# Performance work log

Hardware: AMD Instinct MI355X
Metric: run time of the kernel (lower is better)

The kernel has to match this reference:

```python
import jax, jax.numpy as jnp
import numpy as np

N = 50000      # nodes
E = 800000     # edges (avg degree 16)
G = 500        # graphs in batch
D = 128        # emb_dim
ED = 7         # edge_dim
L = 5          # num_layers
C = 10         # num_class
BN_EPS = 1e-5


def _bn(x, g, b, m, v):
    # BatchNorm1d in eval mode: running stats
    return (x - m) * jax.lax.rsqrt(v + BN_EPS) * g + b


def setup_inputs() -> dict:
    key = jax.random.key(0)
    ks = jax.random.split(key, 32)
    f32 = jnp.float32
    edge_attr = jax.random.normal(ks[0], (E, ED), f32)
    edge_index = jax.random.randint(ks[1], (2, E), 0, N)
    batch = jnp.sort(jax.random.randint(ks[2], (N,), 0, G))

    w = lambda k, shp, s: jax.random.normal(k, shp, f32) * s
    s_in = 1.0 / np.sqrt(D)
    node_emb = w(ks[3], (1, D), 1.0)
    edge_W = w(ks[4], (L, ED, D), 1.0 / np.sqrt(ED))
    edge_b = w(ks[5], (L, D), 0.01)
    mlp_W1 = w(ks[6], (L, D, D), s_in)
    mlp_b1 = w(ks[7], (L, D), 0.01)
    mlp_W2 = w(ks[8], (L, D, D), s_in)
    mlp_b2 = w(ks[9], (L, D), 0.01)
    bn1_g = jax.random.uniform(ks[10], (L, D), f32, 0.5, 1.5)
    bn1_b = w(ks[11], (L, D), 0.1)
    bn1_m = w(ks[12], (L, D), 0.1)
    bn1_v = jax.random.uniform(ks[13], (L, D), f32, 0.5, 1.5)
    bn2_g = jax.random.uniform(ks[14], (L, D), f32, 0.5, 1.5)
    bn2_b = w(ks[15], (L, D), 0.1)
    bn2_m = w(ks[16], (L, D), 0.1)
    bn2_v = jax.random.uniform(ks[17], (L, D), f32, 0.5, 1.5)
    head_W1 = w(ks[18], (D, D), s_in)
    head_b1 = w(ks[19], (D,), 0.01)
    head_W2 = w(ks[20], (D, C), s_in)
    head_b2 = w(ks[21], (C,), 0.01)
    return dict(edge_attr=edge_attr, edge_index=edge_index, batch=batch,
                node_emb=node_emb, edge_W=edge_W, edge_b=edge_b,
                mlp_W1=mlp_W1, mlp_b1=mlp_b1, bn1_g=bn1_g, bn1_b=bn1_b,
                bn1_m=bn1_m, bn1_v=bn1_v, mlp_W2=mlp_W2, mlp_b2=mlp_b2,
                bn2_g=bn2_g, bn2_b=bn2_b, bn2_m=bn2_m, bn2_v=bn2_v,
                head_W1=head_W1, head_b1=head_b1, head_W2=head_W2, head_b2=head_b2)


def reference(edge_attr, edge_index, batch, node_emb, edge_W, edge_b,
              mlp_W1, mlp_b1, bn1_g, bn1_b, bn1_m, bn1_v,
              mlp_W2, mlp_b2, bn2_g, bn2_b, bn2_m, bn2_v,
              head_W1, head_b1, head_W2, head_b2):
    src, dst = edge_index[0], edge_index[1]
    # node_emb indexed by zeros -> every node starts with the same row
    x = jnp.broadcast_to(node_emb[0], (N, D))
    for l in range(L):
        # GINEConv: msg_ij = relu(x_j + Lin(edge_attr_ij)); aggr = sum over in-edges
        e = edge_attr @ edge_W[l] + edge_b[l]               # [E, D]
        msg = jax.nn.relu(x[src] + e)                       # gather + add + relu
        agg = jax.ops.segment_sum(msg, dst, num_segments=N) # scatter-add
        h = x + agg                                         # (1 + eps) * x, eps = 0
        # inner MLP: Linear -> BN -> ReLU -> Linear
        h = h @ mlp_W1[l] + mlp_b1[l]
        h = jax.nn.relu(_bn(h, bn1_g[l], bn1_b[l], bn1_m[l], bn1_v[l]))
        h = h @ mlp_W2[l] + mlp_b2[l]
        # outer BN + ReLU (dropout identity in eval)
        x = jax.nn.relu(_bn(h, bn2_g[l], bn2_b[l], bn2_m[l], bn2_v[l]))
    # global mean pool over graphs
    counts = jnp.maximum(jax.ops.segment_sum(jnp.ones((N,), x.dtype), batch, num_segments=G), 1.0)
    g = jax.ops.segment_sum(x, batch, num_segments=G) / counts[:, None]
    # head: Linear -> ReLU -> (Dropout) -> Linear
    h = jax.nn.relu(g @ head_W1 + head_b1)
    return h @ head_W2 + head_b2
```

## Files before the change

kernel.cpp:

```cpp
#include <hip/hip_runtime.h>

#define N_NODES 50000
#define N_PAD   50048
#define N_EDGES 800000
#define N_GRAPHS 500
#define DIM 128
#define EDIM 7
#define LAYERS 5
#define NCLASS 10
#define BN_EPS 1e-5f
#define TM 64
#define AST 264
#define NSB ((N_NODES + 256) / 256)

typedef __attribute__((ext_vector_type(8))) short bf16x8;
typedef __attribute__((ext_vector_type(4))) float f32x4;
typedef _Float16 h2 __attribute__((ext_vector_type(2)));

__device__ __forceinline__ unsigned short f2bf(float f) {
    unsigned u = __float_as_uint(f);
    u = u + 0x7fffu + ((u >> 16) & 1u);
    return (unsigned short)(u >> 16);
}
__device__ __forceinline__ float bf2f(unsigned short h) {
    return __uint_as_float(((unsigned)h) << 16);
}
__device__ __forceinline__ h2 u2h2(unsigned u) {
    union { unsigned u; h2 h; } c; c.u = u; return c.h;
}
__device__ __forceinline__ unsigned h22u(h2 h) {
    union { h2 h; unsigned u; } c; c.h = h; return c.u;
}
__device__ __forceinline__ unsigned packh2(float a, float b) {
    h2 h; h.x = (_Float16)a; h.y = (_Float16)b;
    return h22u(h);
}


__global__ void zero_ints(int* __restrict__ p, int n) {
    int i = blockIdx.x * 256 + threadIdx.x;
    if (i < n) p[i] = 0;
}

__global__ void hist_kernel(const int* __restrict__ dst, int* __restrict__ deg) {
    int e = blockIdx.x * 256 + threadIdx.x;
    if (e < N_EDGES) atomicAdd(&deg[dst[e]], 1);
}

__global__ __launch_bounds__(256)
void scan1(const int* __restrict__ deg, int* __restrict__ ro, int* __restrict__ bsums) {
    __shared__ int ws[4];
    int t = threadIdx.x;
    int i = blockIdx.x * 256 + t;
    int v = (i < N_NODES) ? deg[i] : 0;
    int lane = t & 63, wv = t >> 6;
    int s = v;
    #pragma unroll
    for (int off = 1; off < 64; off <<= 1) {
        int u = __shfl_up(s, off, 64);
        if (lane >= off) s += u;
    }
    if (lane == 63) ws[wv] = s;
    __syncthreads();
    if (t == 0) {
        int a = 0;
        #pragma unroll
        for (int k = 0; k < 4; ++k) { int x = ws[k]; ws[k] = a; a += x; }
        bsums[blockIdx.x] = a;
    }
    __syncthreads();
    int excl = s - v + ws[wv];
    if (i <= N_NODES) ro[i] = excl;
}

__global__ __launch_bounds__(256)
void scan2(int* __restrict__ bsums) {
    __shared__ int ws[4];
    int t = threadIdx.x;
    int v = (t < NSB) ? bsums[t] : 0;
    int lane = t & 63, wv = t >> 6;
    int s = v;
    #pragma unroll
    for (int off = 1; off < 64; off <<= 1) {
        int u = __shfl_up(s, off, 64);
        if (lane >= off) s += u;
    }
    if (lane == 63) ws[wv] = s;
    __syncthreads();
    if (t == 0) {
        int a = 0;
        #pragma unroll
        for (int k = 0; k < 4; ++k) { int x = ws[k]; ws[k] = a; a += x; }
    }
    __syncthreads();
    if (t < NSB) bsums[t] = s - v + ws[wv];
}

__global__ __launch_bounds__(256)
void scan3(int* __restrict__ ro, const int* __restrict__ bsums, int* __restrict__ cursor) {
    int i = blockIdx.x * 256 + threadIdx.x;
    if (i <= N_NODES) {
        int r = ro[i] + bsums[i >> 8];
        ro[i] = r;
        if (i < N_NODES) cursor[i] = r;
    }
}

__global__ void fill_csr(const int* __restrict__ dst, int* __restrict__ cursor,
                         int* __restrict__ csr_edges) {
    int e = blockIdx.x * 256 + threadIdx.x;
    if (e < N_EDGES) {
        int pos = atomicAdd(&cursor[dst[e]], 1);
        csr_edges[pos] = e;
    }
}


__global__ void init_x(float* __restrict__ x, unsigned short* __restrict__ xb,
                       const float* __restrict__ emb) {
    int i = blockIdx.x * 256 + threadIdx.x;
    if (i < N_NODES * DIM) {
        float v = emb[i & (DIM - 1)];
        x[i] = v;
        xb[i] = f2bf(v);
    }
}

__global__ void prep_ea(const float* __restrict__ ea, _Float16* __restrict__ eah) {
    int i = blockIdx.x * 256 + threadIdx.x;
    if (i < N_EDGES * 8) {
        int e = i >> 3, k = i & 7;
        float v = (k < EDIM) ? ea[e * EDIM + k] : 0.f;
        eah[i] = (_Float16)v;
    }
}

__global__ void prep_w(const float* __restrict__ W1, const float* __restrict__ W2,
                       unsigned short* __restrict__ Wthi, unsigned short* __restrict__ Wtlo) {
    int i = blockIdx.x * 256 + threadIdx.x;
    if (i >= 2 * LAYERS * DIM * DIM) return;
    int m = i >> 14;
    int n = i & 127;
    int k = (i >> 7) & 127;
    const float* W = (m < LAYERS) ? (W1 + (size_t)m * DIM * DIM)
                                  : (W2 + (size_t)(m - LAYERS) * DIM * DIM);
    float v = W[k * DIM + n];
    unsigned short hi = f2bf(v);
    float lo = v - bf2f(hi);
    size_t o = ((size_t)m << 14) + (size_t)n * DIM + k;
    Wthi[o] = hi;
    Wtlo[o] = f2bf(lo);
}


#if __has_builtin(__builtin_amdgcn_fdot2)
#define HAVE_FDOT2 1
#else
#define HAVE_FDOT2 0
#endif

__device__ __forceinline__ void edge_accum(float4& acc, uint4 eav, uint2 xv,
                                           const unsigned* Wp, const float4& bd) {
    float4 el = bd;
#if HAVE_FDOT2
    #pragma unroll
    for (int d = 0; d < 4; ++d) {
        float e = (d == 0) ? el.x : (d == 1) ? el.y : (d == 2) ? el.z : el.w;
        e = __builtin_amdgcn_fdot2(u2h2(eav.x), u2h2(Wp[d * 4 + 0]), e, false);
        e = __builtin_amdgcn_fdot2(u2h2(eav.y), u2h2(Wp[d * 4 + 1]), e, false);
        e = __builtin_amdgcn_fdot2(u2h2(eav.z), u2h2(Wp[d * 4 + 2]), e, false);
        e = __builtin_amdgcn_fdot2(u2h2(eav.w), u2h2(Wp[d * 4 + 3]), e, false);
        if (d == 0) el.x = e; else if (d == 1) el.y = e; else if (d == 2) el.z = e; else el.w = e;
    }
#else
    h2 ea01 = u2h2(eav.x), ea23 = u2h2(eav.y), ea45 = u2h2(eav.z), ea67 = u2h2(eav.w);
    float a[8] = {(float)ea01.x, (float)ea01.y, (float)ea23.x, (float)ea23.y,
                  (float)ea45.x, (float)ea45.y, (float)ea67.x, 0.f};
    #pragma unroll
    for (int d = 0; d < 4; ++d) {
        float e = (d == 0) ? el.x : (d == 1) ? el.y : (d == 2) ? el.z : el.w;
        #pragma unroll
        for (int kp = 0; kp < 4; ++kp) {
            h2 w = u2h2(Wp[d * 4 + kp]);
            e += a[kp * 2] * (float)w.x + a[kp * 2 + 1] * (float)w.y;
        }
        if (d == 0) el.x = e; else if (d == 1) el.y = e; else if (d == 2) el.z = e; else el.w = e;
    }
#endif
    acc.x += fmaxf(__uint_as_float(xv.x << 16)         + el.x, 0.f);
    acc.y += fmaxf(__uint_as_float(xv.x & 0xffff0000u) + el.y, 0.f);
    acc.z += fmaxf(__uint_as_float(xv.y << 16)         + el.z, 0.f);
    acc.w += fmaxf(__uint_as_float(xv.y & 0xffff0000u) + el.w, 0.f);
}

__global__ __launch_bounds__(256, 4)
void aggregate(const float* __restrict__ x, const unsigned short* __restrict__ xb,
               float* __restrict__ h,
               const _Float16* __restrict__ eah,
               const int* __restrict__ srcA,
               const int* __restrict__ csr,
               const int* __restrict__ row_off,
               const float* __restrict__ eW, const float* __restrict__ eb) {
    int t = threadIdx.x;
    int nl = t >> 5, lane = t & 31, c0 = lane * 4;
    int n = blockIdx.x * 8 + nl;

    unsigned Wp[16];
    #pragma unroll
    for (int d = 0; d < 4; ++d) {
        #pragma unroll
        for (int kp = 0; kp < 4; ++kp) {
            float w0 = eW[(kp * 2) * DIM + c0 + d];
            float w1 = (kp * 2 + 1 < EDIM) ? eW[(kp * 2 + 1) * DIM + c0 + d] : 0.f;
            Wp[d * 4 + kp] = packh2(w0, w1);
        }
    }
    float4 bd = *reinterpret_cast<const float4*>(eb + c0);
    #pragma unroll
    for (int k = 0; k < 16; ++k) asm volatile("" : "+v"(Wp[k]));
    asm volatile("" : "+v"(bd.x), "+v"(bd.y), "+v"(bd.z), "+v"(bd.w));

    float4 acc = *reinterpret_cast<const float4*>(x + (size_t)n * DIM + c0);
    int idx = row_off[n], end = row_off[n + 1];

    int e_c[4], s_c[4];
    bool have = (idx + 4 <= end);
    if (have) {
        #pragma unroll
        for (int j = 0; j < 4; ++j) e_c[j] = csr[idx + j];
        #pragma unroll
        for (int j = 0; j < 4; ++j) s_c[j] = srcA[e_c[j]];
    }
    while (have) {
        uint4 ea[4]; uint2 xv[4];
        #pragma unroll
        for (int j = 0; j < 4; ++j) ea[j] = *reinterpret_cast<const uint4*>(eah + (size_t)e_c[j] * 8);
        #pragma unroll
        for (int j = 0; j < 4; ++j) xv[j] = *reinterpret_cast<const uint2*>(xb + (size_t)s_c[j] * DIM + c0);
        idx += 4;
        bool nxt = (idx + 4 <= end);
        int e_n[4], s_n[4];
        if (nxt) {
            #pragma unroll
            for (int j = 0; j < 4; ++j) e_n[j] = csr[idx + j];
            #pragma unroll
            for (int j = 0; j < 4; ++j) s_n[j] = srcA[e_n[j]];
        }
        #pragma unroll
        for (int j = 0; j < 4; ++j) edge_accum(acc, ea[j], xv[j], Wp, bd);
        if (nxt) {
            #pragma unroll
            for (int j = 0; j < 4; ++j) { e_c[j] = e_n[j]; s_c[j] = s_n[j]; }
        }
        have = nxt;
    }
    for (; idx < end; ++idx) {
        int e = csr[idx];
        int s = srcA[e];
        uint4 ea = *reinterpret_cast<const uint4*>(eah + (size_t)e * 8);
        uint2 xv = *reinterpret_cast<const uint2*>(xb + (size_t)s * DIM + c0);
        edge_accum(acc, ea, xv, Wp, bd);
    }
    *reinterpret_cast<float4*>(h + (size_t)n * DIM + c0) = acc;
}


__global__ __launch_bounds__(256)
void gemm2x(const float* __restrict__ in, float* __restrict__ outx,
            unsigned short* __restrict__ xb_out,
            const unsigned short* __restrict__ W1hi, const unsigned short* __restrict__ W1lo,
            const unsigned short* __restrict__ W2hi, const unsigned short* __restrict__ W2lo,
            const float* __restrict__ b1,
            const float* __restrict__ bn1g, const float* __restrict__ bn1b,
            const float* __restrict__ bn1m, const float* __restrict__ bn1v,
            const float* __restrict__ b2,
            const float* __restrict__ bn2g, const float* __restrict__ bn2b,
            const float* __restrict__ bn2m, const float* __restrict__ bn2v) {
    __shared__ __align__(16) unsigned short A2[TM * AST];
    int t = threadIdx.x;
    int r0 = blockIdx.x * TM;
    int w = t >> 6;
    int lane = t & 63;
    int q = lane >> 4;
    int l16 = lane & 15;

    bf16x8 bh[2][4], bl[2][4];
    #pragma unroll
    for (int nt = 0; nt < 2; ++nt) {
        int n = w * 32 + nt * 16 + l16;
        const bf16x8* gh = reinterpret_cast<const bf16x8*>(W1hi + (size_t)n * DIM);
        const bf16x8* gl = reinterpret_cast<const bf16x8*>(W1lo + (size_t)n * DIM);
        #pragma unroll
        for (int kc = 0; kc < 4; ++kc) {
            bh[nt][kc] = gh[kc * 4 + q];
            bl[nt][kc] = gl[kc * 4 + q];
        }
    }

    #pragma unroll
    for (int i = 0; i < 8; ++i) {
        int idx = t + i * 256;
        int row = idx >> 5;
        int kp = (idx & 31) * 4;
        float4 v = reinterpret_cast<const float4*>(in + (size_t)r0 * DIM)[idx];
        unsigned short h0 = f2bf(v.x), h1 = f2bf(v.y), h2_ = f2bf(v.z), h3 = f2bf(v.w);
        ushort4 hv; hv.x = h0; hv.y = h1; hv.z = h2_; hv.w = h3;
        ushort4 lv;
        lv.x = f2bf(v.x - bf2f(h0)); lv.y = f2bf(v.y - bf2f(h1));
        lv.z = f2bf(v.z - bf2f(h2_)); lv.w = f2bf(v.w - bf2f(h3));
        *reinterpret_cast<ushort4*>(&A2[row * AST + kp]) = hv;
        *reinterpret_cast<ushort4*>(&A2[row * AST + 128 + kp]) = lv;
    }
    __syncthreads();

    f32x4 acc[4][2];
    #pragma unroll
    for (int mt = 0; mt < 4; ++mt)
        #pragma unroll
        for (int nt = 0; nt < 2; ++nt)
            acc[mt][nt] = (f32x4){0.f, 0.f, 0.f, 0.f};

    #pragma unroll
    for (int kc = 0; kc < 4; ++kc) {
        bf16x8 ahi[4], alo[4];
        #pragma unroll
        for (int mt = 0; mt < 4; ++mt) {
            ahi[mt] = *reinterpret_cast<const bf16x8*>(&A2[(mt * 16 + l16) * AST + kc * 32 + q * 8]);
            alo[mt] = *reinterpret_cast<const bf16x8*>(&A2[(mt * 16 + l16) * AST + 128 + kc * 32 + q * 8]);
        }
        #pragma unroll
        for (int mt = 0; mt < 4; ++mt)
            #pragma unroll
            for (int nt = 0; nt < 2; ++nt) {
                acc[mt][nt] = __builtin_amdgcn_mfma_f32_16x16x32_bf16(ahi[mt], bh[nt][kc], acc[mt][nt], 0, 0, 0);
                acc[mt][nt] = __builtin_amdgcn_mfma_f32_16x16x32_bf16(ahi[mt], bl[nt][kc], acc[mt][nt], 0, 0, 0);
                acc[mt][nt] = __builtin_amdgcn_mfma_f32_16x16x32_bf16(alo[mt], bh[nt][kc], acc[mt][nt], 0, 0, 0);
            }
    }
    __syncthreads();

    #pragma unroll
    for (int nt = 0; nt < 2; ++nt) {
        int col = w * 32 + nt * 16 + l16;
        float bias = b1[col];
        float sc = bn1g[col] * rsqrtf(bn1v[col] + BN_EPS);
        float sh = bn1b[col] - bn1m[col] * sc;
        #pragma unroll
        for (int mt = 0; mt < 4; ++mt) {
            #pragma unroll
            for (int r = 0; r < 4; ++r) {
                int rowl = mt * 16 + q * 4 + r;
                float o = fmaxf((acc[mt][nt][r] + bias) * sc + sh, 0.f);
                unsigned short hi = f2bf(o);
                A2[rowl * AST + col] = hi;
                A2[rowl * AST + 128 + col] = f2bf(o - bf2f(hi));
            }
        }
    }

    #pragma unroll
    for (int nt = 0; nt < 2; ++nt) {
        int n = w * 32 + nt * 16 + l16;
        const bf16x8* gh = reinterpret_cast<const bf16x8*>(W2hi + (size_t)n * DIM);
        const bf16x8* gl = reinterpret_cast<const bf16x8*>(W2lo + (size_t)n * DIM);
        #pragma unroll
        for (int kc = 0; kc < 4; ++kc) {
            bh[nt][kc] = gh[kc * 4 + q];
            bl[nt][kc] = gl[kc * 4 + q];
        }
    }
    __syncthreads();

    #pragma unroll
    for (int mt = 0; mt < 4; ++mt)
        #pragma unroll
        for (int nt = 0; nt < 2; ++nt)
            acc[mt][nt] = (f32x4){0.f, 0.f, 0.f, 0.f};

    #pragma unroll
    for (int kc = 0; kc < 4; ++kc) {
        bf16x8 ahi[4], alo[4];
        #pragma unroll
        for (int mt = 0; mt < 4; ++mt) {
            ahi[mt] = *reinterpret_cast<const bf16x8*>(&A2[(mt * 16 + l16) * AST + kc * 32 + q * 8]);
            alo[mt] = *reinterpret_cast<const bf16x8*>(&A2[(mt * 16 + l16) * AST + 128 + kc * 32 + q * 8]);
        }
        #pragma unroll
        for (int mt = 0; mt < 4; ++mt)
            #pragma unroll
            for (int nt = 0; nt < 2; ++nt) {
                acc[mt][nt] = __builtin_amdgcn_mfma_f32_16x16x32_bf16(ahi[mt], bh[nt][kc], acc[mt][nt], 0, 0, 0);
                acc[mt][nt] = __builtin_amdgcn_mfma_f32_16x16x32_bf16(ahi[mt], bl[nt][kc], acc[mt][nt], 0, 0, 0);
                acc[mt][nt] = __builtin_amdgcn_mfma_f32_16x16x32_bf16(alo[mt], bh[nt][kc], acc[mt][nt], 0, 0, 0);
            }
    }

    #pragma unroll
    for (int nt = 0; nt < 2; ++nt) {
        int col = w * 32 + nt * 16 + l16;
        float bias = b2[col];
        float sc = bn2g[col] * rsqrtf(bn2v[col] + BN_EPS);
        float sh = bn2b[col] - bn2m[col] * sc;
        #pragma unroll
        for (int mt = 0; mt < 4; ++mt) {
            #pragma unroll
            for (int r = 0; r < 4; ++r) {
                int row = r0 + mt * 16 + q * 4 + r;
                float o = fmaxf((acc[mt][nt][r] + bias) * sc + sh, 0.f);
                outx[(size_t)row * DIM + col] = o;
                xb_out[(size_t)row * DIM + col] = f2bf(o);
            }
        }
    }
}


__global__ __launch_bounds__(256)
void pool_kernel(const float* __restrict__ x, const int* __restrict__ batch,
                 float* __restrict__ g) {
    __shared__ float sh[256];
    __shared__ int sb[2];
    int gid = blockIdx.x;
    int t = threadIdx.x;
    if (t < 2) {
        int tgt = gid + t;
        int lo = 0, hi = N_NODES;
        while (lo < hi) { int mid = (lo + hi) >> 1; if (batch[mid] < tgt) lo = mid + 1; else hi = mid; }
        sb[t] = lo;
    }
    __syncthreads();
    int lo = sb[0], hi = sb[1];
    int d = t & 127, half = t >> 7;
    float a = 0.f;
    for (int n = lo + half; n < hi; n += 2) a += x[(size_t)n * DIM + d];
    sh[t] = a;
    __syncthreads();
    if (t < DIM) {
        float cnt = fmaxf((float)(hi - lo), 1.f);
        g[gid * DIM + t] = (sh[t] + sh[t + 128]) / cnt;
    }
}


__global__ __launch_bounds__(128)
void head1_kernel(const float* __restrict__ g, const float* __restrict__ W1,
                  const float* __restrict__ b1, float* __restrict__ h1) {
    __shared__ float gs[DIM];
    int gid = blockIdx.x, c = threadIdx.x;
    gs[c] = g[gid * DIM + c];
    __syncthreads();
    float acc = b1[c];
    for (int k = 0; k < DIM; ++k) acc += gs[k] * W1[k * DIM + c];
    h1[gid * DIM + c] = fmaxf(acc, 0.f);
}

__global__ __launch_bounds__(64)
void head2_kernel(const float* __restrict__ h1, const float* __restrict__ W2,
                  const float* __restrict__ b2, float* __restrict__ out) {
    __shared__ float hs[DIM];
    int gid = blockIdx.x;
    int t = threadIdx.x;
    hs[t] = h1[gid * DIM + t];
    hs[t + 64] = h1[gid * DIM + t + 64];
    __syncthreads();
    if (t < NCLASS) {
        float acc = b2[t];
        for (int k = 0; k < DIM; ++k) acc += hs[k] * W2[k * NCLASS + t];
        out[gid * NCLASS + t] = acc;
    }
}


extern "C" void kernel_launch(void* const* d_in, const int* in_sizes, int n_in,
                              void* d_out, int out_size, void* d_ws, size_t ws_size,
                              hipStream_t stream) {
    const float* edge_attr = (const float*)d_in[0];
    const int*   edge_index = (const int*)d_in[1];
    const int*   batch = (const int*)d_in[2];
    const float* node_emb = (const float*)d_in[3];
    const float* edge_W = (const float*)d_in[4];
    const float* edge_b = (const float*)d_in[5];
    const float* mlp_W1 = (const float*)d_in[6];
    const float* mlp_b1 = (const float*)d_in[7];
    const float* bn1_g = (const float*)d_in[8];
    const float* bn1_b = (const float*)d_in[9];
    const float* bn1_m = (const float*)d_in[10];
    const float* bn1_v = (const float*)d_in[11];
    const float* mlp_W2 = (const float*)d_in[12];
    const float* mlp_b2 = (const float*)d_in[13];
    const float* bn2_g = (const float*)d_in[14];
    const float* bn2_b = (const float*)d_in[15];
    const float* bn2_m = (const float*)d_in[16];
    const float* bn2_v = (const float*)d_in[17];
    const float* head_W1 = (const float*)d_in[18];
    const float* head_b1 = (const float*)d_in[19];
    const float* head_W2 = (const float*)d_in[20];
    const float* head_b2 = (const float*)d_in[21];
    float* out = (float*)d_out;

    const int* src = edge_index;
    const int* dst = edge_index + N_EDGES;

    size_t off = 0;
    auto carve = [&](size_t bytes) {
        void* p = (char*)d_ws + off;
        off += (bytes + 255) & ~(size_t)255;
        return p;
    };
    float* x            = (float*)carve((size_t)N_PAD * DIM * 4);
    unsigned short* xb  = (unsigned short*)carve((size_t)N_PAD * DIM * 2);
    float* h            = (float*)carve((size_t)N_PAD * DIM * 4);
    _Float16* eah       = (_Float16*)carve((size_t)N_EDGES * 8 * 2);
    unsigned short* Wthi = (unsigned short*)carve((size_t)2 * LAYERS * DIM * DIM * 2);
    unsigned short* Wtlo = (unsigned short*)carve((size_t)2 * LAYERS * DIM * DIM * 2);
    int* deg      = (int*)carve((size_t)N_NODES * 4);
    int* row_off  = (int*)carve((size_t)(N_NODES + 1) * 4);
    int* cursor   = (int*)carve((size_t)N_NODES * 4);
    int* csr      = (int*)carve((size_t)N_EDGES * 4);
    int* bsums    = (int*)carve((size_t)NSB * 4);
    float* gbuf   = (float*)carve((size_t)N_GRAPHS * DIM * 4);
    float* h1buf  = (float*)carve((size_t)N_GRAPHS * DIM * 4);
    (void)ws_size;

    zero_ints<<<(N_NODES + 255) / 256, 256, 0, stream>>>(deg, N_NODES);
    hist_kernel<<<(N_EDGES + 255) / 256, 256, 0, stream>>>(dst, deg);
    scan1<<<NSB, 256, 0, stream>>>(deg, row_off, bsums);
    scan2<<<1, 256, 0, stream>>>(bsums);
    scan3<<<NSB, 256, 0, stream>>>(row_off, bsums, cursor);
    fill_csr<<<(N_EDGES + 255) / 256, 256, 0, stream>>>(dst, cursor, csr);

    init_x<<<(N_NODES * DIM + 255) / 256, 256, 0, stream>>>(x, xb, node_emb);
    prep_ea<<<(N_EDGES * 8 + 255) / 256, 256, 0, stream>>>(edge_attr, eah);
    prep_w<<<(2 * LAYERS * DIM * DIM + 255) / 256, 256, 0, stream>>>(mlp_W1, mlp_W2, Wthi, Wtlo);

    const int gemm_blocks = N_PAD / TM;
    for (int l = 0; l < LAYERS; ++l) {
        aggregate<<<N_NODES / 8, 256, 0, stream>>>(
            x, xb, h, eah, src, csr, row_off,
            edge_W + (size_t)l * EDIM * DIM, edge_b + (size_t)l * DIM);
        gemm2x<<<gemm_blocks, 256, 0, stream>>>(
            h, x, xb,
            Wthi + ((size_t)l << 14), Wtlo + ((size_t)l << 14),
            Wthi + ((size_t)(LAYERS + l) << 14), Wtlo + ((size_t)(LAYERS + l) << 14),
            mlp_b1 + (size_t)l * DIM,
            bn1_g + (size_t)l * DIM, bn1_b + (size_t)l * DIM,
            bn1_m + (size_t)l * DIM, bn1_v + (size_t)l * DIM,
            mlp_b2 + (size_t)l * DIM,
            bn2_g + (size_t)l * DIM, bn2_b + (size_t)l * DIM,
            bn2_m + (size_t)l * DIM, bn2_v + (size_t)l * DIM);
    }

    pool_kernel<<<N_GRAPHS, 256, 0, stream>>>(x, batch, gbuf);
    head1_kernel<<<N_GRAPHS, 128, 0, stream>>>(gbuf, head_W1, head_b1, h1buf);
    head2_kernel<<<N_GRAPHS, 64, 0, stream>>>(h1buf, head_W2, head_b2, out);
}
```

Baseline: 712.6 us.

## Pre-permute edge attrs and sources into CSR order to remove indirection

Adds a one-time kernel that reorders the edge source indices and half-precision edge attributes into CSR (destination-sorted) order. The per-layer aggregate kernel then reads both contiguously by position instead of going through csr then src or eah, removing one dependent random load per edge in all five layers. It also raises the aggregate occupancy hint from 4 to 6 and hoists the W2 weight loads in gemm2x ahead of the BN1 epilogue. The cost is an extra prep pass plus about 16 MB of workspace, and the higher occupancy target may force register spilling.

```diff
diff --git a/kernel.cpp b/kernel.cpp
--- a/kernel.cpp
+++ b/kernel.cpp
@@ -132,6 +132,18 @@
         int e = i >> 3, k = i & 7;
         float v = (k < EDIM) ? ea[e * EDIM + k] : 0.f;
         eah[i] = (_Float16)v;
+    }
+}
+
+__global__ void prep_perm(const int* __restrict__ csr, const int* __restrict__ src,
+                          const _Float16* __restrict__ eah,
+                          int* __restrict__ srcc, _Float16* __restrict__ eac) {
+    int i = blockIdx.x * 256 + threadIdx.x;
+    if (i < N_EDGES) {
+        int e = csr[i];
+        srcc[i] = src[e];
+        *reinterpret_cast<uint4*>(eac + (size_t)i * 8) =
+            *reinterpret_cast<const uint4*>(eah + (size_t)e * 8);
     }
 }
 
@@ -193,12 +205,11 @@
     acc.w += fmaxf(__uint_as_float(xv.y & 0xffff0000u) + el.w, 0.f);
 }
 
-__global__ __launch_bounds__(256, 4)
+__global__ __launch_bounds__(256, 6)
 void aggregate(const float* __restrict__ x, const unsigned short* __restrict__ xb,
                float* __restrict__ h,
-               const _Float16* __restrict__ eah,
-               const int* __restrict__ srcA,
-               const int* __restrict__ csr,
+               const _Float16* __restrict__ eac,
+               const int* __restrict__ srcc,
                const int* __restrict__ row_off,
                const float* __restrict__ eW, const float* __restrict__ eb) {
     int t = threadIdx.x;
@@ -223,41 +234,36 @@
     float4 acc = *reinterpret_cast<const float4*>(x + (size_t)n * DIM + c0);
     int idx = row_off[n], end = row_off[n + 1];
 
-    int e_c[4], s_c[4];
+    int s_c[4];
     bool have = (idx + 4 <= end);
     if (have) {
         #pragma unroll
-        for (int j = 0; j < 4; ++j) e_c[j] = csr[idx + j];
-        #pragma unroll
-        for (int j = 0; j < 4; ++j) s_c[j] = srcA[e_c[j]];
+        for (int j = 0; j < 4; ++j) s_c[j] = srcc[idx + j];
     }
     while (have) {
         uint4 ea[4]; uint2 xv[4];
         #pragma unroll
-        for (int j = 0; j < 4; ++j) ea[j] = *reinterpret_cast<const uint4*>(eah + (size_t)e_c[j] * 8);
+        for (int j = 0; j < 4; ++j) ea[j] = *reinterpret_cast<const uint4*>(eac + (size_t)(idx + j) * 8);
         #pragma unroll
         for (int j = 0; j < 4; ++j) xv[j] = *reinterpret_cast<const uint2*>(xb + (size_t)s_c[j] * DIM + c0);
         idx += 4;
         bool nxt = (idx + 4 <= end);
-        int e_n[4], s_n[4];
+        int s_n[4];
         if (nxt) {
             #pragma unroll
-            for (int j = 0; j < 4; ++j) e_n[j] = csr[idx + j];
-            #pragma unroll
-            for (int j = 0; j < 4; ++j) s_n[j] = srcA[e_n[j]];
+            for (int j = 0; j < 4; ++j) s_n[j] = srcc[idx + j];
         }
         #pragma unroll
         for (int j = 0; j < 4; ++j) edge_accum(acc, ea[j], xv[j], Wp, bd);
         if (nxt) {
             #pragma unroll
-            for (int j = 0; j < 4; ++j) { e_c[j] = e_n[j]; s_c[j] = s_n[j]; }
+            for (int j = 0; j < 4; ++j) s_c[j] = s_n[j];
         }
         have = nxt;
     }
     for (; idx < end; ++idx) {
-        int e = csr[idx];
-        int s = srcA[e];
-        uint4 ea = *reinterpret_cast<const uint4*>(eah + (size_t)e * 8);
+        int s = srcc[idx];
+        uint4 ea = *reinterpret_cast<const uint4*>(eac + (size_t)idx * 8);
         uint2 xv = *reinterpret_cast<const uint2*>(xb + (size_t)s * DIM + c0);
         edge_accum(acc, ea, xv, Wp, bd);
     }
@@ -341,6 +347,18 @@
 
     #pragma unroll
     for (int nt = 0; nt < 2; ++nt) {
+        int n = w * 32 + nt * 16 + l16;
+        const bf16x8* gh = reinterpret_cast<const bf16x8*>(W2hi + (size_t)n * DIM);
+        const bf16x8* gl = reinterpret_cast<const bf16x8*>(W2lo + (size_t)n * DIM);
+        #pragma unroll
+        for (int kc = 0; kc < 4; ++kc) {
+            bh[nt][kc] = gh[kc * 4 + q];
+            bl[nt][kc] = gl[kc * 4 + q];
+        }
+    }
+
+    #pragma unroll
+    for (int nt = 0; nt < 2; ++nt) {
         int col = w * 32 + nt * 16 + l16;
         float bias = b1[col];
         float sc = bn1g[col] * rsqrtf(bn1v[col] + BN_EPS);
@@ -355,18 +373,6 @@
                 A2[rowl * AST + col] = hi;
                 A2[rowl * AST + 128 + col] = f2bf(o - bf2f(hi));
             }
-        }
-    }
-
-    #pragma unroll
-    for (int nt = 0; nt < 2; ++nt) {
-        int n = w * 32 + nt * 16 + l16;
-        const bf16x8* gh = reinterpret_cast<const bf16x8*>(W2hi + (size_t)n * DIM);
-        const bf16x8* gl = reinterpret_cast<const bf16x8*>(W2lo + (size_t)n * DIM);
-        #pragma unroll
-        for (int kc = 0; kc < 4; ++kc) {
-            bh[nt][kc] = gh[kc * 4 + q];
-            bl[nt][kc] = gl[kc * 4 + q];
         }
     }
     __syncthreads();
@@ -511,6 +517,8 @@
     unsigned short* xb  = (unsigned short*)carve((size_t)N_PAD * DIM * 2);
     float* h            = (float*)carve((size_t)N_PAD * DIM * 4);
     _Float16* eah       = (_Float16*)carve((size_t)N_EDGES * 8 * 2);
+    _Float16* eac       = (_Float16*)carve((size_t)N_EDGES * 8 * 2);
+    int* srcc           = (int*)carve((size_t)N_EDGES * 4);
     unsigned short* Wthi = (unsigned short*)carve((size_t)2 * LAYERS * DIM * DIM * 2);
     unsigned short* Wtlo = (unsigned short*)carve((size_t)2 * LAYERS * DIM * DIM * 2);
     int* deg      = (int*)carve((size_t)N_NODES * 4);
@@ -531,12 +539,13 @@
 
     init_x<<<(N_NODES * DIM + 255) / 256, 256, 0, stream>>>(x, xb, node_emb);
     prep_ea<<<(N_EDGES * 8 + 255) / 256, 256, 0, stream>>>(edge_attr, eah);
+    prep_perm<<<(N_EDGES + 255) / 256, 256, 0, stream>>>(csr, src, eah, srcc, eac);
     prep_w<<<(2 * LAYERS * DIM * DIM + 255) / 256, 256, 0, stream>>>(mlp_W1, mlp_W2, Wthi, Wtlo);
 
     const int gemm_blocks = N_PAD / TM;
     for (int l = 0; l < LAYERS; ++l) {
         aggregate<<<N_NODES / 8, 256, 0, stream>>>(
-            x, xb, h, eah, src, csr, row_off,
+            x, xb, h, eac, srcc, row_off,
             edge_W + (size_t)l * EDIM * DIM, edge_b + (size_t)l * DIM);
         gemm2x<<<gemm_blocks, 256, 0, stream>>>(
             h, x, xb,
```

New measurement: 652.6 us. -8.4%, faster.

## Pack edge attrs and src into CSR-ordered records; widen aggregate to 8 cols/thread

Applied to the files above, without the earlier changes.

Builds a 32-byte per-edge record in CSR order holding the fp16 edge attributes and the source index. This replaces the separate csr→edge-id→src→attr indirection chain with one contiguous read per edge, and it also drops the prep_ea kernel. The aggregate kernel now uses 16 threads per node with 8 columns each. That halves the redundant per-edge record loads across lanes and widens the gathers to 16 bytes, at the cost of more registers (32 packed weights). In the GEMM, the W2 loads are moved before the BN1 epilogue so their latency overlaps it.

```diff
diff --git a/kernel.cpp b/kernel.cpp
--- a/kernel.cpp
+++ b/kernel.cpp
@@ -12,10 +12,13 @@
 #define TM 64
 #define AST 264
 #define NSB ((N_NODES + 256) / 256)
+#define NBA 16
 
 typedef __attribute__((ext_vector_type(8))) short bf16x8;
 typedef __attribute__((ext_vector_type(4))) float f32x4;
 typedef _Float16 h2 __attribute__((ext_vector_type(2)));
+
+struct __align__(32) ERec { uint4 ea; int src; int pad0, pad1, pad2; };
 
 __device__ __forceinline__ unsigned short f2bf(float f) {
     unsigned u = __float_as_uint(f);
@@ -106,12 +109,21 @@
     }
 }
 
-__global__ void fill_csr(const int* __restrict__ dst, int* __restrict__ cursor,
-                         int* __restrict__ csr_edges) {
+__global__ void fill_rec(const int* __restrict__ dst, const int* __restrict__ src,
+                         const float* __restrict__ edge_attr,
+                         int* __restrict__ cursor, ERec* __restrict__ rec) {
     int e = blockIdx.x * 256 + threadIdx.x;
     if (e < N_EDGES) {
+        const float* ap = edge_attr + (size_t)e * EDIM;
+        uint4 ea;
+        ea.x = packh2(ap[0], ap[1]);
+        ea.y = packh2(ap[2], ap[3]);
+        ea.z = packh2(ap[4], ap[5]);
+        ea.w = packh2(ap[6], 0.f);
+        int s = src[e];
         int pos = atomicAdd(&cursor[dst[e]], 1);
-        csr_edges[pos] = e;
+        rec[pos].ea = ea;
+        rec[pos].src = s;
     }
 }
 
@@ -123,15 +135,6 @@
         float v = emb[i & (DIM - 1)];
         x[i] = v;
         xb[i] = f2bf(v);
-    }
-}
-
-__global__ void prep_ea(const float* __restrict__ ea, _Float16* __restrict__ eah) {
-    int i = blockIdx.x * 256 + threadIdx.x;
-    if (i < N_EDGES * 8) {
-        int e = i >> 3, k = i & 7;
-        float v = (k < EDIM) ? ea[e * EDIM + k] : 0.f;
-        eah[i] = (_Float16)v;
     }
 }
 
@@ -159,55 +162,59 @@
 #define HAVE_FDOT2 0
 #endif
 
-__device__ __forceinline__ void edge_accum(float4& acc, uint4 eav, uint2 xv,
-                                           const unsigned* Wp, const float4& bd) {
-    float4 el = bd;
+__device__ __forceinline__ void edge_accum8(float4& acc0, float4& acc1,
+                                            uint4 eav, uint4 xv,
+                                            const unsigned* Wp,
+                                            const float4& b0, const float4& b1) {
+    float el[8] = {b0.x, b0.y, b0.z, b0.w, b1.x, b1.y, b1.z, b1.w};
 #if HAVE_FDOT2
     #pragma unroll
-    for (int d = 0; d < 4; ++d) {
-        float e = (d == 0) ? el.x : (d == 1) ? el.y : (d == 2) ? el.z : el.w;
+    for (int d = 0; d < 8; ++d) {
+        float e = el[d];
         e = __builtin_amdgcn_fdot2(u2h2(eav.x), u2h2(Wp[d * 4 + 0]), e, false);
         e = __builtin_amdgcn_fdot2(u2h2(eav.y), u2h2(Wp[d * 4 + 1]), e, false);
         e = __builtin_amdgcn_fdot2(u2h2(eav.z), u2h2(Wp[d * 4 + 2]), e, false);
         e = __builtin_amdgcn_fdot2(u2h2(eav.w), u2h2(Wp[d * 4 + 3]), e, false);
-        if (d == 0) el.x = e; else if (d == 1) el.y = e; else if (d == 2) el.z = e; else el.w = e;
+        el[d] = e;
     }
 #else
     h2 ea01 = u2h2(eav.x), ea23 = u2h2(eav.y), ea45 = u2h2(eav.z), ea67 = u2h2(eav.w);
     float a[8] = {(float)ea01.x, (float)ea01.y, (float)ea23.x, (float)ea23.y,
                   (float)ea45.x, (float)ea45.y, (float)ea67.x, 0.f};
     #pragma unroll
-    for (int d = 0; d < 4; ++d) {
-        float e = (d == 0) ? el.x : (d == 1) ? el.y : (d == 2) ? el.z : el.w;
+    for (int d = 0; d < 8; ++d) {
+        float e = el[d];
         #pragma unroll
         for (int kp = 0; kp < 4; ++kp) {
             h2 w = u2h2(Wp[d * 4 + kp]);
             e += a[kp * 2] * (float)w.x + a[kp * 2 + 1] * (float)w.y;
         }
-        if (d == 0) el.x = e; else if (d == 1) el.y = e; else if (d == 2) el.z = e; else el.w = e;
+        el[d] = e;
     }
 #endif
-    acc.x += fmaxf(__uint_as_float(xv.x << 16)         + el.x, 0.f);
-    acc.y += fmaxf(__uint_as_float(xv.x & 0xffff0000u) + el.y, 0.f);
-    acc.z += fmaxf(__uint_as_float(xv.y << 16)         + el.z, 0.f);
-    acc.w += fmaxf(__uint_as_float(xv.y & 0xffff0000u) + el.w, 0.f);
+    acc0.x += fmaxf(__uint_as_float(xv.x << 16)         + el[0], 0.f);
+    acc0.y += fmaxf(__uint_as_float(xv.x & 0xffff0000u) + el[1], 0.f);
+    acc0.z += fmaxf(__uint_as_float(xv.y << 16)         + el[2], 0.f);
+    acc0.w += fmaxf(__uint_as_float(xv.y & 0xffff0000u) + el[3], 0.f);
+    acc1.x += fmaxf(__uint_as_float(xv.z << 16)         + el[4], 0.f);
+    acc1.y += fmaxf(__uint_as_float(xv.z & 0xffff0000u) + el[5], 0.f);
+    acc1.z += fmaxf(__uint_as_float(xv.w << 16)         + el[6], 0.f);
+    acc1.w += fmaxf(__uint_as_float(xv.w & 0xffff0000u) + el[7], 0.f);
 }
 
 __global__ __launch_bounds__(256, 4)
 void aggregate(const float* __restrict__ x, const unsigned short* __restrict__ xb,
                float* __restrict__ h,
-               const _Float16* __restrict__ eah,
-               const int* __restrict__ srcA,
-               const int* __restrict__ csr,
+               const ERec* __restrict__ rec,
                const int* __restrict__ row_off,
                const float* __restrict__ eW, const float* __restrict__ eb) {
     int t = threadIdx.x;
-    int nl = t >> 5, lane = t & 31, c0 = lane * 4;
-    int n = blockIdx.x * 8 + nl;
-
-    unsigned Wp[16];
-    #pragma unroll
-    for (int d = 0; d < 4; ++d) {
+    int nl = t >> 4, lane = t & 15, c0 = lane * 8;
+    int n = blockIdx.x * NBA + nl;
+
+    unsigned Wp[32];
+    #pragma unroll
+    for (int d = 0; d < 8; ++d) {
         #pragma unroll
         for (int kp = 0; kp < 4; ++kp) {
             float w0 = eW[(kp * 2) * DIM + c0 + d];
@@ -215,53 +222,52 @@
             Wp[d * 4 + kp] = packh2(w0, w1);
         }
     }
-    float4 bd = *reinterpret_cast<const float4*>(eb + c0);
-    #pragma unroll
-    for (int k = 0; k < 16; ++k) asm volatile("" : "+v"(Wp[k]));
-    asm volatile("" : "+v"(bd.x), "+v"(bd.y), "+v"(bd.z), "+v"(bd.w));
-
-    float4 acc = *reinterpret_cast<const float4*>(x + (size_t)n * DIM + c0);
+    float4 b0 = *reinterpret_cast<const float4*>(eb + c0);
+    float4 b1 = *reinterpret_cast<const float4*>(eb + c0 + 4);
+    #pragma unroll
+    for (int k = 0; k < 32; ++k) asm volatile("" : "+v"(Wp[k]));
+    asm volatile("" : "+v"(b0.x), "+v"(b0.y), "+v"(b0.z), "+v"(b0.w));
+    asm volatile("" : "+v"(b1.x), "+v"(b1.y), "+v"(b1.z), "+v"(b1.w));
+
+    float4 acc0 = *reinterpret_cast<const float4*>(x + (size_t)n * DIM + c0);
+    float4 acc1 = *reinterpret_cast<const float4*>(x + (size_t)n * DIM + c0 + 4);
     int idx = row_off[n], end = row_off[n + 1];
 
-    int e_c[4], s_c[4];
+    int s_c[4];
     bool have = (idx + 4 <= end);
     if (have) {
         #pragma unroll
-        for (int j = 0; j < 4; ++j) e_c[j] = csr[idx + j];
-        #pragma unroll
-        for (int j = 0; j < 4; ++j) s_c[j] = srcA[e_c[j]];
+        for (int j = 0; j < 4; ++j) s_c[j] = rec[idx + j].src;
     }
     while (have) {
-        uint4 ea[4]; uint2 xv[4];
-        #pragma unroll
-        for (int j = 0; j < 4; ++j) ea[j] = *reinterpret_cast<const uint4*>(eah + (size_t)e_c[j] * 8);
-        #pragma unroll
-        for (int j = 0; j < 4; ++j) xv[j] = *reinterpret_cast<const uint2*>(xb + (size_t)s_c[j] * DIM + c0);
+        uint4 ea[4], xv[4];
+        #pragma unroll
+        for (int j = 0; j < 4; ++j) ea[j] = rec[idx + j].ea;
+        #pragma unroll
+        for (int j = 0; j < 4; ++j) xv[j] = *reinterpret_cast<const uint4*>(xb + (size_t)s_c[j] * DIM + c0);
         idx += 4;
         bool nxt = (idx + 4 <= end);
-        int e_n[4], s_n[4];
+        int s_n[4];
         if (nxt) {
             #pragma unroll
-            for (int j = 0; j < 4; ++j) e_n[j] = csr[idx + j];
-            #pragma unroll
-            for (int j = 0; j < 4; ++j) s_n[j] = srcA[e_n[j]];
-        }
-        #pragma unroll
-        for (int j = 0; j < 4; ++j) edge_accum(acc, ea[j], xv[j], Wp, bd);
+            for (int j = 0; j < 4; ++j) s_n[j] = rec[idx + j].src;
+        }
+        #pragma unroll
+        for (int j = 0; j < 4; ++j) edge_accum8(acc0, acc1, ea[j], xv[j], Wp, b0, b1);
         if (nxt) {
             #pragma unroll
-            for (int j = 0; j < 4; ++j) { e_c[j] = e_n[j]; s_c[j] = s_n[j]; }
+            for (int j = 0; j < 4; ++j) s_c[j] = s_n[j];
         }
         have = nxt;
     }
     for (; idx < end; ++idx) {
-        int e = csr[idx];
-        int s = srcA[e];
-        uint4 ea = *reinterpret_cast<const uint4*>(eah + (size_t)e * 8);
-        uint2 xv = *reinterpret_cast<const uint2*>(xb + (size_t)s * DIM + c0);
-        edge_accum(acc, ea, xv, Wp, bd);
-    }
-    *reinterpret_cast<float4*>(h + (size_t)n * DIM + c0) = acc;
+        int s = rec[idx].src;
+        uint4 ea = rec[idx].ea;
+        uint4 xv = *reinterpret_cast<const uint4*>(xb + (size_t)s * DIM + c0);
+        edge_accum8(acc0, acc1, ea, xv, Wp, b0, b1);
+    }
+    *reinterpret_cast<float4*>(h + (size_t)n * DIM + c0) = acc0;
+    *reinterpret_cast<float4*>(h + (size_t)n * DIM + c0 + 4) = acc1;
 }
 
 
@@ -341,6 +347,18 @@
 
     #pragma unroll
     for (int nt = 0; nt < 2; ++nt) {
+        int n = w * 32 + nt * 16 + l16;
+        const bf16x8* gh = reinterpret_cast<const bf16x8*>(W2hi + (size_t)n * DIM);
+        const bf16x8* gl = reinterpret_cast<const bf16x8*>(W2lo + (size_t)n * DIM);
+        #pragma unroll
+        for (int kc = 0; kc < 4; ++kc) {
+            bh[nt][kc] = gh[kc * 4 + q];
+            bl[nt][kc] = gl[kc * 4 + q];
+        }
+    }
+
+    #pragma unroll
+    for (int nt = 0; nt < 2; ++nt) {
         int col = w * 32 + nt * 16 + l16;
         float bias = b1[col];
         float sc = bn1g[col] * rsqrtf(bn1v[col] + BN_EPS);
@@ -355,18 +373,6 @@
                 A2[rowl * AST + col] = hi;
                 A2[rowl * AST + 128 + col] = f2bf(o - bf2f(hi));
             }
-        }
-    }
-
-    #pragma unroll
-    for (int nt = 0; nt < 2; ++nt) {
-        int n = w * 32 + nt * 16 + l16;
-        const bf16x8* gh = reinterpret_cast<const bf16x8*>(W2hi + (size_t)n * DIM);
-        const bf16x8* gl = reinterpret_cast<const bf16x8*>(W2lo + (size_t)n * DIM);
-        #pragma unroll
-        for (int kc = 0; kc < 4; ++kc) {
-            bh[nt][kc] = gh[kc * 4 + q];
-            bl[nt][kc] = gl[kc * 4 + q];
         }
     }
     __syncthreads();
@@ -510,13 +516,12 @@
     float* x            = (float*)carve((size_t)N_PAD * DIM * 4);
     unsigned short* xb  = (unsigned short*)carve((size_t)N_PAD * DIM * 2);
     float* h            = (float*)carve((size_t)N_PAD * DIM * 4);
-    _Float16* eah       = (_Float16*)carve((size_t)N_EDGES * 8 * 2);
+    ERec* rec           = (ERec*)carve((size_t)N_EDGES * sizeof(ERec));
     unsigned short* Wthi = (unsigned short*)carve((size_t)2 * LAYERS * DIM * DIM * 2);
     unsigned short* Wtlo = (unsigned short*)carve((size_t)2 * LAYERS * DIM * DIM * 2);
     int* deg      = (int*)carve((size_t)N_NODES * 4);
     int* row_off  = (int*)carve((size_t)(N_NODES + 1) * 4);
     int* cursor   = (int*)carve((size_t)N_NODES * 4);
-    int* csr      = (int*)carve((size_t)N_EDGES * 4);
     int* bsums    = (int*)carve((size_t)NSB * 4);
     float* gbuf   = (float*)carve((size_t)N_GRAPHS * DIM * 4);
     float* h1buf  = (float*)carve((size_t)N_GRAPHS * DIM * 4);
@@ -527,16 +532,15 @@
     scan1<<<NSB, 256, 0, stream>>>(deg, row_off, bsums);
     scan2<<<1, 256, 0, stream>>>(bsums);
     scan3<<<NSB, 256, 0, stream>>>(row_off, bsums, cursor);
-    fill_csr<<<(N_EDGES + 255) / 256, 256, 0, stream>>>(dst, cursor, csr);
+    fill_rec<<<(N_EDGES + 255) / 256, 256, 0, stream>>>(dst, src, edge_attr, cursor, rec);
 
     init_x<<<(N_NODES * DIM + 255) / 256, 256, 0, stream>>>(x, xb, node_emb);
-    prep_ea<<<(N_EDGES * 8 + 255) / 256, 256, 0, stream>>>(edge_attr, eah);
     prep_w<<<(2 * LAYERS * DIM * DIM + 255) / 256, 256, 0, stream>>>(mlp_W1, mlp_W2, Wthi, Wtlo);
 
     const int gemm_blocks = N_PAD / TM;
     for (int l = 0; l < LAYERS; ++l) {
-        aggregate<<<N_NODES / 8, 256, 0, stream>>>(
-            x, xb, h, eah, src, csr, row_off,
+        aggregate<<<N_NODES / NBA, 256, 0, stream>>>(
+            x, xb, h, rec, row_off,
             edge_W + (size_t)l * EDIM * DIM, edge_b + (size_t)l * DIM);
         gemm2x<<<gemm_blocks, 256, 0, stream>>>(
             h, x, xb,
```

Result: faster. 606.6 us (-14.9%).
